# Performance work log

Hardware: AMD Instinct MI355X
Metric: run time of the kernel (lower is better)

## Reference

```python
import jax, jax.numpy as jnp
import numpy as np

B, C, H, W = 32, 512, 32, 32
CI = C // 2  # inter_channels
EPS = 1e-5


def setup_inputs() -> dict:
    key = jax.random.key(0)
    ks = jax.random.split(key, 12)
    s = 0.02
    return {
        "x": jax.random.normal(ks[0], (B, C, H, W), jnp.float32),
        "w_g": jax.random.normal(ks[1], (CI, C), jnp.float32) * s,
        "b_g": jax.random.normal(ks[2], (CI,), jnp.float32) * s,
        "w_theta": jax.random.normal(ks[3], (CI, C), jnp.float32) * s,
        "b_theta": jax.random.normal(ks[4], (CI,), jnp.float32) * s,
        "w_phi": jax.random.normal(ks[5], (CI, C), jnp.float32) * s,
        "b_phi": jax.random.normal(ks[6], (CI,), jnp.float32) * s,
        "w_W": jax.random.normal(ks[7], (C, CI), jnp.float32) * s,
        "b_W": jax.random.normal(ks[8], (C,), jnp.float32) * s,
        "bn_gamma": jax.random.normal(ks[9], (C,), jnp.float32) * 0.1 + 1.0,
        "bn_beta": jax.random.normal(ks[10], (C,), jnp.float32) * 0.1,
        "bn_mean": jax.random.normal(ks[11], (C,), jnp.float32) * 0.1,
        "bn_var": jnp.abs(jax.random.normal(jax.random.fold_in(key, 99), (C,), jnp.float32)) * 0.5 + 0.5,
    }


def reference(x, w_g, b_g, w_theta, b_theta, w_phi, b_phi, w_W, b_W,
              bn_gamma, bn_beta, bn_mean, bn_var):
    b, c, h, w = x.shape
    n = h * w
    xf = x.reshape(b, c, n)  # [B, C, N]
    # 1x1 convs == per-pixel channel matmuls
    g = jnp.einsum('oc,bcn->bon', w_g, xf) + b_g[:, None]          # [B, Ci, N]
    theta = jnp.einsum('oc,bcn->bon', w_theta, xf) + b_theta[:, None]
    phi = jnp.einsum('oc,bcn->bon', w_phi, xf) + b_phi[:, None]
    # f[b, i, j] = theta_i . phi_j ; scaled by 1/N (softmax-free attention)
    f_div_C = jnp.einsum('bcn,bcm->bnm', theta, phi) / n           # [B, N, N]
    # y[b, c, n] = sum_m f[b, n, m] * g[b, c, m]
    y = jnp.einsum('bnm,bcm->bcn', f_div_C, g)                     # [B, Ci, N]
    # W: 1x1 conv back to C channels + BatchNorm (inference form)
    Wy = jnp.einsum('oi,bin->bon', w_W, y) + b_W[:, None]          # [B, C, N]
    inv_std = jax.lax.rsqrt(bn_var + EPS)
    bn = (Wy - bn_mean[:, None]) * (inv_std * bn_gamma)[:, None] + bn_beta[:, None]
    z = bn.reshape(b, c, h, w) + x
    return z
```

## Files before the change

### kernel.cpp

```cpp
#include <hip/hip_runtime.h>
#include <hip/hip_bf16.h>
#include <cstdint>
#include <cstddef>

using bf16 = __hip_bfloat16;
typedef __attribute__((ext_vector_type(8))) short short8v;
typedef __attribute__((ext_vector_type(4))) float f32x4;

static constexpr int BATCH = 32;
static constexpr int CH    = 512;
static constexpr int CIc   = 256;
static constexpr int NSP   = 1024;
#define EPSV 1e-5f

__device__ __forceinline__ bf16 f2bf(float f) { return __float2bfloat16(f); }

__device__ __forceinline__ void gload_lds16(const bf16* g, bf16* l) {
  __builtin_amdgcn_global_load_lds(
      (const __attribute__((address_space(1))) void*)g,
      (__attribute__((address_space(3))) void*)l, 16, 0, 0);
}

__global__ __launch_bounds__(256) void convert_weights(
    const float* __restrict__ wg, const float* __restrict__ wph, const float* __restrict__ wth,
    const float* __restrict__ bg, const float* __restrict__ bph, const float* __restrict__ bth,
    const float* __restrict__ wW,
    bf16* __restrict__ wcat, bf16* __restrict__ wWb, float* __restrict__ biascat)
{
  int i = blockIdx.x * 256 + threadIdx.x;
  const int WSZ = CIc * CH;
  if (i < WSZ) {
    wcat[i]         = f2bf(wg[i]);
    wcat[WSZ + i]   = f2bf(wph[i]);
    wcat[2*WSZ + i] = f2bf(wth[i]);
    wWb[i]          = f2bf(wW[i]);
  }
  if (i < CIc) {
    biascat[i]        = bg[i];
    biascat[CIc + i]  = bph[i];
    biascat[2*CIc + i]= bth[i];
  }
}

__global__ __launch_bounds__(256) void transpose_x_kernel(
    const float* __restrict__ x, bf16* __restrict__ xt)
{
  __shared__ bf16 t[32][34];
  int n0 = blockIdx.x * 32, c0 = blockIdx.y * 32, b = blockIdx.z;
  const float* s = x + (size_t)b * CH * NSP;
  bf16* d = xt + (size_t)b * NSP * CH;
  int tx = threadIdx.x & 31, ty = threadIdx.x >> 5;
  #pragma unroll
  for (int i = 0; i < 32; i += 8)
    t[ty + i][tx] = f2bf(s[(size_t)(c0 + ty + i) * NSP + n0 + tx]);
  __syncthreads();
  #pragma unroll
  for (int i = 0; i < 32; i += 8)
    d[(size_t)(n0 + ty + i) * CH + c0 + tx] = t[tx][ty + i];
}

template<int EPI>
__global__ __launch_bounds__(512, 2) void gemm_nt_256(
    const bf16* __restrict__ A, size_t sA,
    const bf16* __restrict__ Bm, size_t sB,
    void* __restrict__ Cm,
    int K,
    const float* __restrict__ bias,
    bf16* __restrict__ Tt,
    const float* __restrict__ bW, const float* __restrict__ gma,
    const float* __restrict__ bta, const float* __restrict__ mu,
    const float* __restrict__ var,
    const float* __restrict__ xres)
{
  __shared__ bf16 As[3][16 * 512];
  __shared__ bf16 Bs[3][16 * 512];
  const int zb = blockIdx.z;
  const int m0 = blockIdx.y * 256;
  const int n0 = blockIdx.x * 256;
  const bf16* Ab = A  + (size_t)zb * sA;
  const bf16* Bb = Bm + (size_t)zb * sB;
  const int tid  = threadIdx.x;
  const int wv   = tid >> 6, lane = tid & 63;
  const int l16  = lane & 15, g4 = lane >> 4;
  const int wr   = wv >> 2,  wc = wv & 3;

  f32x4 acc[8][4];
  #pragma unroll
  for (int i = 0; i < 8; ++i)
    #pragma unroll
    for (int j = 0; j < 4; ++j)
      acc[i][j] = (f32x4){0.f, 0.f, 0.f, 0.f};

  auto SA = [&](int tt) {
    int s = tt % 3;
    int kbase = tt * 32 + g4 * 8;
    #pragma unroll
    for (int q = 0; q < 2; ++q) {
      int f = wv * 2 + q;
      gload_lds16(Ab + (size_t)(m0 + f * 16 + l16) * K + kbase, &As[s][f * 512]);
    }
  };
  auto SB = [&](int tt) {
    int s = tt % 3;
    int kbase = tt * 32 + g4 * 8;
    #pragma unroll
    for (int q = 0; q < 2; ++q) {
      int f = wv * 2 + q;
      gload_lds16(Bb + (size_t)(n0 + f * 16 + l16) * K + kbase, &Bs[s][f * 512]);
    }
  };

  const int nt = K >> 5;
  SA(0); SB(0); SA(1); SB(1);
  asm volatile("s_waitcnt vmcnt(4)" ::: "memory");
  __builtin_amdgcn_s_barrier();

  for (int t = 0; t < nt; ++t) {
    const int s = t % 3;
    short8v af[4], bfr[4];
    #pragma unroll
    for (int mf = 0; mf < 4; ++mf)
      af[mf] = *(const short8v*)&As[s][(wr * 8 + mf) * 512 + lane * 8];
    #pragma unroll
    for (int nf = 0; nf < 4; ++nf)
      bfr[nf] = *(const short8v*)&Bs[s][(wc * 4 + nf) * 512 + lane * 8];
    if (t + 2 < nt) SA(t + 2);
    asm volatile("s_waitcnt lgkmcnt(0)" ::: "memory");
    __builtin_amdgcn_sched_barrier(0);
    __builtin_amdgcn_s_setprio(1);
    #pragma unroll
    for (int mf = 0; mf < 4; ++mf)
      #pragma unroll
      for (int nf = 0; nf < 4; ++nf)
        acc[mf][nf] = __builtin_amdgcn_mfma_f32_16x16x32_bf16(af[mf], bfr[nf], acc[mf][nf], 0, 0, 0);
    __builtin_amdgcn_s_setprio(0);

    short8v af2[4];
    #pragma unroll
    for (int mf = 0; mf < 4; ++mf)
      af2[mf] = *(const short8v*)&As[s][(wr * 8 + 4 + mf) * 512 + lane * 8];
    if (t + 2 < nt) SB(t + 2);
    asm volatile("s_waitcnt lgkmcnt(0)" ::: "memory");
    __builtin_amdgcn_sched_barrier(0);
    __builtin_amdgcn_s_setprio(1);
    #pragma unroll
    for (int mf = 0; mf < 4; ++mf)
      #pragma unroll
      for (int nf = 0; nf < 4; ++nf)
        acc[4 + mf][nf] = __builtin_amdgcn_mfma_f32_16x16x32_bf16(af2[mf], bfr[nf], acc[4 + mf][nf], 0, 0, 0);
    __builtin_amdgcn_s_setprio(0);

    if (t + 1 < nt) {
      if (t + 2 < nt) asm volatile("s_waitcnt vmcnt(4)" ::: "memory");
      else            asm volatile("s_waitcnt vmcnt(0)" ::: "memory");
      __builtin_amdgcn_s_barrier();
    }
  }

  const int colbase = n0 + wc * 64 + l16;
  const int rowb    = wr * 128 + g4 * 4;

  if constexpr (EPI == 2) {
    #pragma unroll
    for (int mf = 0; mf < 8; ++mf) {
      #pragma unroll
      for (int j = 0; j < 4; ++j) {
        int row = m0 + rowb + mf * 16 + j;
        float a  = gma[row] * rsqrtf(var[row] + EPSV);
        float bb = (bW[row] - mu[row]) * a + bta[row];
        float sc = a * (1.f / (float)NSP);
        #pragma unroll
        for (int nf = 0; nf < 4; ++nf) {
          int col = colbase + nf * 16;
          size_t idx = (size_t)zb * (CH * NSP) + (size_t)row * NSP + col;
          ((float*)Cm)[idx] = acc[mf][nf][j] * sc + bb + ((const float*)xres)[idx];
        }
      }
    }
  } else {
    if (m0 < 512) {
      #pragma unroll
      for (int mf = 0; mf < 8; ++mf)
        #pragma unroll
        for (int j = 0; j < 4; ++j) {
          int row = m0 + rowb + mf * 16 + j;
          float badd = bias[row];
          #pragma unroll
          for (int nf = 0; nf < 4; ++nf) {
            int col = colbase + nf * 16;
            int b = col >> 10, n = col & 1023;
            ((bf16*)Cm)[(size_t)b * (CH * NSP) + (size_t)row * NSP + n] = f2bf(acc[mf][nf][j] + badd);
          }
        }
    } else {
      #pragma unroll
      for (int mf = 0; mf < 8; ++mf) {
        int ci0 = rowb + mf * 16;
        #pragma unroll
        for (int nf = 0; nf < 4; ++nf) {
          int col = colbase + nf * 16;
          int b = col >> 10, n = col & 1023;
          uint64_t pk = 0;
          #pragma unroll
          for (int j = 0; j < 4; ++j) {
            bf16 bv = f2bf(acc[mf][nf][j] + bias[512 + ci0 + j]);
            pk |= (uint64_t)(*(unsigned short*)&bv) << (16 * j);
          }
          *(uint64_t*)(Tt + (size_t)b * (NSP * CIc) + (size_t)n * CIc + ci0) = pk;
        }
      }
    }
  }
}

__global__ __launch_bounds__(256) void gemm_nt_small(
    const bf16* __restrict__ A, size_t sA,
    const bf16* __restrict__ Bm, size_t sB,
    bf16* __restrict__ Cm, size_t sC,
    int N, int K)
{
  __shared__ bf16 As[2][128 * 64];
  __shared__ bf16 Bs[2][128 * 64];
  const int b  = blockIdx.z;
  const int m0 = blockIdx.y * 128;
  const int n0 = blockIdx.x * 128;
  const bf16* Ab = A  + (size_t)b * sA;
  const bf16* Bb = Bm + (size_t)b * sB;
  const int tid  = threadIdx.x;
  const int wv   = tid >> 6, lane = tid & 63;
  const int l16  = lane & 15, g4 = lane >> 4;
  const int wr   = wv >> 1,  wc = wv & 1;

  f32x4 acc[4][4];
  #pragma unroll
  for (int i = 0; i < 4; ++i)
    #pragma unroll
    for (int j = 0; j < 4; ++j)
      acc[i][j] = (f32x4){0.f, 0.f, 0.f, 0.f};

  auto stage = [&](int ks, int p) {
    #pragma unroll
    for (int i = 0; i < 4; ++i) {
      int s = i * 256 + tid;
      int row = s >> 3, ch8 = (s & 7) << 3;
      gload_lds16(Ab + (size_t)(m0 + row) * K + ks + ch8, &As[p][(i * 256 + wv * 64) * 8]);
      gload_lds16(Bb + (size_t)(n0 + row) * K + ks + ch8, &Bs[p][(i * 256 + wv * 64) * 8]);
    }
  };

  const int nt = K >> 6;
  stage(0, 0);
  __syncthreads();
  for (int t = 0; t < nt; ++t) {
    const int cur = t & 1;
    if (t + 1 < nt) stage((t + 1) << 6, cur ^ 1);
    #pragma unroll
    for (int kk = 0; kk < 2; ++kk) {
      short8v af[4], bfv[4];
      #pragma unroll
      for (int mf = 0; mf < 4; ++mf)
        af[mf] = *(const short8v*)&As[cur][(wr * 64 + mf * 16 + l16) * 64 + kk * 32 + g4 * 8];
      #pragma unroll
      for (int nf = 0; nf < 4; ++nf)
        bfv[nf] = *(const short8v*)&Bs[cur][(wc * 64 + nf * 16 + l16) * 64 + kk * 32 + g4 * 8];
      #pragma unroll
      for (int mf = 0; mf < 4; ++mf)
        #pragma unroll
        for (int nf = 0; nf < 4; ++nf)
          acc[mf][nf] = __builtin_amdgcn_mfma_f32_16x16x32_bf16(af[mf], bfv[nf], acc[mf][nf], 0, 0, 0);
    }
    __syncthreads();
  }

  const int colbase = n0 + wc * 64 + l16;
  const int rowbase = m0 + wr * 64 + g4 * 4;
  #pragma unroll
  for (int mf = 0; mf < 4; ++mf)
    #pragma unroll
    for (int j = 0; j < 4; ++j) {
      int row = rowbase + mf * 16 + j;
      #pragma unroll
      for (int nf = 0; nf < 4; ++nf) {
        int col = colbase + nf * 16;
        Cm[(size_t)b * sC + (size_t)row * N + col] = f2bf(acc[mf][nf][j]);
      }
    }
}

extern "C" void kernel_launch(void* const* d_in, const int* in_sizes, int n_in,
                              void* d_out, int out_size, void* d_ws, size_t ws_size,
                              hipStream_t stream)
{
  const float* x    = (const float*)d_in[0];
  const float* w_g  = (const float*)d_in[1];
  const float* b_g  = (const float*)d_in[2];
  const float* w_th = (const float*)d_in[3];
  const float* b_th = (const float*)d_in[4];
  const float* w_ph = (const float*)d_in[5];
  const float* b_ph = (const float*)d_in[6];
  const float* w_W  = (const float*)d_in[7];
  const float* b_W  = (const float*)d_in[8];
  const float* gma  = (const float*)d_in[9];
  const float* bta  = (const float*)d_in[10];
  const float* mu   = (const float*)d_in[11];
  const float* var  = (const float*)d_in[12];
  float* out = (float*)d_out;

  char* ws = (char*)d_ws;
  bf16* proj = (bf16*)(ws + 0);
  bf16* xt   = (bf16*)(ws + 33554432);
  bf16* thT  = (bf16*)(ws + 67108864);
  bf16* S    = (bf16*)(ws + 83886080);
  bf16* T    = (bf16*)(ws + 88080384);
  bf16* wcat = (bf16*)(ws + 96468992);
  bf16* wWb  = (bf16*)(ws + 97255424);
  float* bcat= (float*)(ws + 97517568);

  convert_weights<<<512, 256, 0, stream>>>(w_g, w_ph, w_th, b_g, b_ph, b_th, w_W, wcat, wWb, bcat);
  transpose_x_kernel<<<dim3(32, 16, 32), 256, 0, stream>>>(x, xt);

  gemm_nt_256<1><<<dim3(128, 3, 1), 512, 0, stream>>>(
      wcat, 0, xt, 0, proj, CH, bcat, thT,
      nullptr, nullptr, nullptr, nullptr, nullptr, nullptr);

  gemm_nt_small<<<dim3(2, 2, 32), 256, 0, stream>>>(
      proj + 256 * 1024, (size_t)CH * NSP, proj, (size_t)CH * NSP, S, (size_t)CIc * CIc,
      CIc, NSP);

  gemm_nt_small<<<dim3(2, 4, 32), 256, 0, stream>>>(
      wWb, 0, S, (size_t)CIc * CIc, T, (size_t)CH * CIc,
      CIc, CIc);

  gemm_nt_256<2><<<dim3(4, 2, 32), 512, 0, stream>>>(
      T, (size_t)CH * CIc, thT, (size_t)NSP * CIc, out, CIc,
      nullptr, nullptr, b_W, gma, bta, mu, var, x);
}
```

Before: 141.5 us.

## Shrink GEMM tile to 256x128 with swizzled LDS and double buffering

```diff
diff --git a/kernel.cpp b/kernel.cpp
--- a/kernel.cpp
+++ b/kernel.cpp
@@ -60,7 +60,7 @@
 }
 
 template<int EPI>
-__global__ __launch_bounds__(512, 2) void gemm_nt_256(
+__global__ __launch_bounds__(512, 4) void gemm_bt(
     const bf16* __restrict__ A, size_t sA,
     const bf16* __restrict__ Bm, size_t sB,
     void* __restrict__ Cm,
@@ -72,97 +72,72 @@
     const float* __restrict__ var,
     const float* __restrict__ xres)
 {
-  __shared__ bf16 As[3][16 * 512];
-  __shared__ bf16 Bs[3][16 * 512];
-  const int zb = blockIdx.z;
-  const int m0 = blockIdx.y * 256;
-  const int n0 = blockIdx.x * 256;
+  __shared__ bf16 As[2][256 * 32];
+  __shared__ bf16 Bs[2][128 * 32];
+  int m0, n0, zb;
+  if constexpr (EPI == 1) {
+    int bidx = blockIdx.x;
+    int wg = (bidx & 7) * 96 + (bidx >> 3);
+    m0 = (wg >> 8) * 256;
+    n0 = (wg & 255) * 128;
+    zb = 0;
+  } else {
+    m0 = blockIdx.y * 256; n0 = blockIdx.x * 128; zb = blockIdx.z;
+  }
   const bf16* Ab = A  + (size_t)zb * sA;
   const bf16* Bb = Bm + (size_t)zb * sB;
   const int tid  = threadIdx.x;
   const int wv   = tid >> 6, lane = tid & 63;
   const int l16  = lane & 15, g4 = lane >> 4;
-  const int wr   = wv >> 2,  wc = wv & 3;
-
-  f32x4 acc[8][4];
-  #pragma unroll
-  for (int i = 0; i < 8; ++i)
+  const int wr   = wv >> 1,  wc = wv & 1;
+
+  f32x4 acc[4][4];
+  #pragma unroll
+  for (int i = 0; i < 4; ++i)
     #pragma unroll
     for (int j = 0; j < 4; ++j)
       acc[i][j] = (f32x4){0.f, 0.f, 0.f, 0.f};
 
-  auto SA = [&](int tt) {
-    int s = tt % 3;
-    int kbase = tt * 32 + g4 * 8;
-    #pragma unroll
-    for (int q = 0; q < 2; ++q) {
-      int f = wv * 2 + q;
-      gload_lds16(Ab + (size_t)(m0 + f * 16 + l16) * K + kbase, &As[s][f * 512]);
-    }
+  const int rq  = lane >> 2;
+  const int oct = (lane & 3) ^ ((lane >> 3) & 3);
+  auto stage = [&](int t, int p) {
+    int kb = t * 32 + oct * 8;
+    #pragma unroll
+    for (int i = 0; i < 2; ++i) {
+      int f = wv * 2 + i;
+      gload_lds16(Ab + (size_t)(m0 + f * 16 + rq) * K + kb, &As[p][f * 512]);
+    }
+    gload_lds16(Bb + (size_t)(n0 + wv * 16 + rq) * K + kb, &Bs[p][wv * 512]);
   };
-  auto SB = [&](int tt) {
-    int s = tt % 3;
-    int kbase = tt * 32 + g4 * 8;
-    #pragma unroll
-    for (int q = 0; q < 2; ++q) {
-      int f = wv * 2 + q;
-      gload_lds16(Bb + (size_t)(n0 + f * 16 + l16) * K + kbase, &Bs[s][f * 512]);
-    }
-  };
-
+
+  const int rs = (g4 ^ ((l16 >> 1) & 3)) * 8;
   const int nt = K >> 5;
-  SA(0); SB(0); SA(1); SB(1);
-  asm volatile("s_waitcnt vmcnt(4)" ::: "memory");
-  __builtin_amdgcn_s_barrier();
-
+  stage(0, 0);
+  __syncthreads();
   for (int t = 0; t < nt; ++t) {
-    const int s = t % 3;
-    short8v af[4], bfr[4];
+    const int cur = t & 1;
+    if (t + 1 < nt) stage(t + 1, cur ^ 1);
+    short8v af[4], bfv[4];
     #pragma unroll
     for (int mf = 0; mf < 4; ++mf)
-      af[mf] = *(const short8v*)&As[s][(wr * 8 + mf) * 512 + lane * 8];
+      af[mf] = *(const short8v*)&As[cur][(wr * 64 + mf * 16 + l16) * 32 + rs];
     #pragma unroll
     for (int nf = 0; nf < 4; ++nf)
-      bfr[nf] = *(const short8v*)&Bs[s][(wc * 4 + nf) * 512 + lane * 8];
-    if (t + 2 < nt) SA(t + 2);
-    asm volatile("s_waitcnt lgkmcnt(0)" ::: "memory");
-    __builtin_amdgcn_sched_barrier(0);
-    __builtin_amdgcn_s_setprio(1);
+      bfv[nf] = *(const short8v*)&Bs[cur][(wc * 64 + nf * 16 + l16) * 32 + rs];
     #pragma unroll
     for (int mf = 0; mf < 4; ++mf)
       #pragma unroll
       for (int nf = 0; nf < 4; ++nf)
-        acc[mf][nf] = __builtin_amdgcn_mfma_f32_16x16x32_bf16(af[mf], bfr[nf], acc[mf][nf], 0, 0, 0);
-    __builtin_amdgcn_s_setprio(0);
-
-    short8v af2[4];
-    #pragma unroll
-    for (int mf = 0; mf < 4; ++mf)
-      af2[mf] = *(const short8v*)&As[s][(wr * 8 + 4 + mf) * 512 + lane * 8];
-    if (t + 2 < nt) SB(t + 2);
-    asm volatile("s_waitcnt lgkmcnt(0)" ::: "memory");
-    __builtin_amdgcn_sched_barrier(0);
-    __builtin_amdgcn_s_setprio(1);
-    #pragma unroll
-    for (int mf = 0; mf < 4; ++mf)
-      #pragma unroll
-      for (int nf = 0; nf < 4; ++nf)
-        acc[4 + mf][nf] = __builtin_amdgcn_mfma_f32_16x16x32_bf16(af2[mf], bfr[nf], acc[4 + mf][nf], 0, 0, 0);
-    __builtin_amdgcn_s_setprio(0);
-
-    if (t + 1 < nt) {
-      if (t + 2 < nt) asm volatile("s_waitcnt vmcnt(4)" ::: "memory");
-      else            asm volatile("s_waitcnt vmcnt(0)" ::: "memory");
-      __builtin_amdgcn_s_barrier();
-    }
+        acc[mf][nf] = __builtin_amdgcn_mfma_f32_16x16x32_bf16(af[mf], bfv[nf], acc[mf][nf], 0, 0, 0);
+    __syncthreads();
   }
 
   const int colbase = n0 + wc * 64 + l16;
-  const int rowb    = wr * 128 + g4 * 4;
+  const int rowb    = wr * 64 + g4 * 4;
 
   if constexpr (EPI == 2) {
     #pragma unroll
-    for (int mf = 0; mf < 8; ++mf) {
+    for (int mf = 0; mf < 4; ++mf) {
       #pragma unroll
       for (int j = 0; j < 4; ++j) {
         int row = m0 + rowb + mf * 16 + j;
@@ -180,7 +155,7 @@
   } else {
     if (m0 < 512) {
       #pragma unroll
-      for (int mf = 0; mf < 8; ++mf)
+      for (int mf = 0; mf < 4; ++mf)
         #pragma unroll
         for (int j = 0; j < 4; ++j) {
           int row = m0 + rowb + mf * 16 + j;
@@ -194,7 +169,7 @@
         }
     } else {
       #pragma unroll
-      for (int mf = 0; mf < 8; ++mf) {
+      for (int mf = 0; mf < 4; ++mf) {
         int ci0 = rowb + mf * 16;
         #pragma unroll
         for (int nf = 0; nf < 4; ++nf) {
@@ -319,7 +294,7 @@
   convert_weights<<<512, 256, 0, stream>>>(w_g, w_ph, w_th, b_g, b_ph, b_th, w_W, wcat, wWb, bcat);
   transpose_x_kernel<<<dim3(32, 16, 32), 256, 0, stream>>>(x, xt);
 
-  gemm_nt_256<1><<<dim3(128, 3, 1), 512, 0, stream>>>(
+  gemm_bt<1><<<dim3(768, 1, 1), 512, 0, stream>>>(
       wcat, 0, xt, 0, proj, CH, bcat, thT,
       nullptr, nullptr, nullptr, nullptr, nullptr, nullptr);
 
@@ -331,7 +306,7 @@
       wWb, 0, S, (size_t)CIc * CIc, T, (size_t)CH * CIc,
       CIc, CIc);
 
-  gemm_nt_256<2><<<dim3(4, 2, 32), 512, 0, stream>>>(
+  gemm_bt<2><<<dim3(8, 2, 32), 512, 0, stream>>>(
       T, (size_t)CH * CIc, thT, (size_t)NSP * CIc, out, CIc,
       nullptr, nullptr, b_W, gma, bta, mu, var, x);
 }
```

After: 132.1 us. 6.6% less time.
